# Kernel tuning notes

Measured on AMD Instinct MI355X. Metric: run time of the kernel, lower is better.

## Reference

```python
import jax, jax.numpy as jnp
import numpy as np

WS = 7      # window size
SS = 3      # shift size
NH = 6      # num heads
C = 192     # dim
B = 32
HH = 112
WW = 112


def _rel_pos_index(ws):
    coords = np.stack(np.meshgrid(np.arange(ws), np.arange(ws), indexing='ij'))
    cf = coords.reshape(2, -1)
    rel = (cf[:, :, None] - cf[:, None, :]).transpose(1, 2, 0)
    rel[:, :, 0] += ws - 1
    rel[:, :, 1] += ws - 1
    rel[:, :, 0] *= 2 * ws - 1
    return rel.sum(-1)  # (N, N) int


def _attn_mask(H, W, ws, ss):
    # standard Swin SW-MSA mask: -100 where tokens come from different regions
    img = np.zeros((H, W))
    cnt = 0
    for h in (slice(0, -ws), slice(-ws, -ss), slice(-ss, None)):
        for w in (slice(0, -ws), slice(-ws, -ss), slice(-ss, None)):
            img[h, w] = cnt
            cnt += 1
    mw = img.reshape(H // ws, ws, W // ws, ws).transpose(0, 2, 1, 3).reshape(-1, ws * ws)
    diff = mw[:, None, :] - mw[:, :, None]
    return np.where(diff != 0, -100.0, 0.0).astype(np.float32)  # (nW, N, N)


def _ln(x, g, b, eps=1e-5):
    m = x.mean(-1, keepdims=True)
    v = ((x - m) ** 2).mean(-1, keepdims=True)
    return (x - m) * jax.lax.rsqrt(v + eps) * g + b


def setup_inputs() -> dict:
    key = jax.random.key(0)
    ks = jax.random.split(key, 8)
    hid = 4 * C
    nbias = (2 * WS - 1) * (2 * WS - 1)
    return {
        'x': jax.random.normal(ks[0], (B, HH * WW, C), dtype=jnp.float32),
        'norm1_g': jnp.ones((C,), jnp.float32),
        'norm1_b': jnp.zeros((C,), jnp.float32),
        'qkv_w': jax.random.normal(ks[1], (3 * C, C), jnp.float32) * 0.02,
        'qkv_b': jnp.zeros((3 * C,), jnp.float32),
        'rpb_table': jax.random.normal(ks[2], (nbias, NH), jnp.float32) * 0.02,
        'proj_w': jax.random.normal(ks[3], (C, C), jnp.float32) * 0.02,
        'proj_b': jnp.zeros((C,), jnp.float32),
        'norm2_g': jnp.ones((C,), jnp.float32),
        'norm2_b': jnp.zeros((C,), jnp.float32),
        'fc1_w': jax.random.normal(ks[4], (hid, C), jnp.float32) * 0.02,
        'fc1_b': jnp.zeros((hid,), jnp.float32),
        'fc2_w': jax.random.normal(ks[5], (C, hid), jnp.float32) * 0.02,
        'fc2_b': jnp.zeros((C,), jnp.float32),
        'H': HH,
        'W': WW,
    }


def reference(x, norm1_g, norm1_b, qkv_w, qkv_b, rpb_table, proj_w, proj_b,
              norm2_g, norm2_b, fc1_w, fc1_b, fc2_w, fc2_b, H, W):
    Bb, L, Cc = x.shape
    N = WS * WS
    hd = Cc // NH
    rpi = jnp.asarray(_rel_pos_index(WS))                      # (N, N)
    amask = jnp.asarray(_attn_mask(H, W, WS, SS))              # (nW, N, N)
    nW = amask.shape[0]

    shortcut = x
    h = _ln(x, norm1_g, norm1_b).reshape(Bb, H, W, Cc)
    # cyclic shift
    h = jnp.roll(h, shift=(-SS, -SS), axis=(1, 2))
    # window partition -> (B*nW, N, C)
    h = h.reshape(Bb, H // WS, WS, W // WS, WS, Cc).transpose(0, 1, 3, 2, 4, 5)
    xw = h.reshape(-1, N, Cc)
    Bn = xw.shape[0]

    qkv = (xw @ qkv_w.T + qkv_b).reshape(Bn, N, 3, NH, hd).transpose(2, 0, 3, 1, 4)
    q, k, v = qkv[0], qkv[1], qkv[2]                           # (Bn, NH, N, hd)
    q = q * (hd ** -0.5)
    attn = jnp.einsum('bhnd,bhmd->bhnm', q, k)                 # (Bn, NH, N, N)
    bias = rpb_table[rpi.reshape(-1)].reshape(N, N, NH).transpose(2, 0, 1)
    attn = attn + bias[None]
    attn = (attn.reshape(Bb, nW, NH, N, N) + amask[None, :, None]).reshape(Bn, NH, N, N)
    attn = jax.nn.softmax(attn, axis=-1)
    out = jnp.einsum('bhnm,bhmd->bhnd', attn, v).transpose(0, 2, 1, 3).reshape(Bn, N, Cc)
    out = out @ proj_w.T + proj_b

    # window reverse + reverse cyclic shift
    out = out.reshape(Bb, H // WS, W // WS, WS, WS, Cc).transpose(0, 1, 3, 2, 4, 5).reshape(Bb, H, W, Cc)
    out = jnp.roll(out, shift=(SS, SS), axis=(1, 2)).reshape(Bb, L, Cc)

    x = shortcut + out
    y = _ln(x, norm2_g, norm2_b)
    y = jax.nn.gelu(y @ fc1_w.T + fc1_b, approximate=False) @ fc2_w.T + fc2_b
    return x + y
```

## Files before the change

### kernel.cpp

```cpp
#include <hip/hip_runtime.h>
#include <stdint.h>
#include <math.h>


typedef unsigned short u16;
typedef unsigned int   u32;
typedef __bf16 v8bf __attribute__((ext_vector_type(8)));
typedef float  v4f  __attribute__((ext_vector_type(4)));
typedef u16    v8u16 __attribute__((ext_vector_type(8)));
typedef u16    v4u16 __attribute__((ext_vector_type(4)));

#define MFMA16(a,b,c) __builtin_amdgcn_mfma_f32_16x16x32_bf16(a,b,c,0,0,0)

#define HSTR 77070336L
#define QSC  0.17677669529663687f

__device__ __forceinline__ u16 f2bf(float f){
  return __builtin_bit_cast(u16, (__bf16)f);
}

__device__ __forceinline__ void async16(void* lds, const void* g){
  __builtin_amdgcn_global_load_lds(
      (__attribute__((address_space(1))) void*)(g),
      (__attribute__((address_space(3))) void*)(lds), 16, 0, 0);
}

__global__ __launch_bounds__(256)
void convw(const float* __restrict__ s0, const float* __restrict__ s1,
           const float* __restrict__ s2, const float* __restrict__ s3,
           u16* __restrict__ d){
  int i = blockIdx.x * 256 + threadIdx.x;
  float v;
  if (i < 110592){
    v = s0[i];
    if (i < 36864) v *= QSC;
  }
  else if (i < 147456)  v = s1[i - 110592];
  else if (i < 294912)  v = s2[i - 147456];
  else                  v = s3[i - 294912];
  d[i] = f2bf(v);
}

__global__ __launch_bounds__(256)
void bmt_k(const float* __restrict__ rpb, float* __restrict__ bmt){
  int idx = blockIdx.x * 256 + threadIdx.x;
  int r  = idx & 3, lg = (idx >> 2) & 3, lr = (idx >> 4) & 15;
  int n  = (idx >> 8) & 3, m = (idx >> 10) & 3;
  int t  = idx >> 12; int h = t % 6, cls = t / 6;
  int row = m*16 + lg*4 + r, col = n*16 + lr;
  float v;
  if (row >= 49 || col >= 49){
    v = -1e30f;
  } else {
    int i1 = row / 7, j1 = row - i1 * 7;
    int i2 = col / 7, j2 = col - i2 * 7;
    int ridx = (i1 - i2 + 6) * 13 + (j1 - j2 + 6);
    v = rpb[ridx * 6 + h];
    int lh1 = (cls & 2) ? (i1 < 4 ? 1 : 2) : 0;
    int lw1 = (cls & 1) ? (j1 < 4 ? 1 : 2) : 0;
    int lh2 = (cls & 2) ? (i2 < 4 ? 1 : 2) : 0;
    int lw2 = (cls & 1) ? (j2 < 4 ? 1 : 2) : 0;
    if (lh1 * 3 + lw1 != lh2 * 3 + lw2) v -= 100.f;
  }
  bmt[idx] = v;
}

template<bool GATHER>
__global__ __launch_bounds__(256)
void ln_kern(const float* __restrict__ x, const float* __restrict__ g,
             const float* __restrict__ b, u16* __restrict__ o){
  const int ts  = threadIdx.x >> 4;
  const int l16 = threadIdx.x & 15;
  const int r   = blockIdx.x * 16 + ts;
  const float* src;
  if (GATHER){
    u32 wdx = (u32)r / 49u; int nn = r - (int)wdx * 49;
    int bb = (int)(wdx >> 8); int wl = (int)(wdx & 255);
    int wh = wl >> 4, wwi = wl & 15;
    int ii = (int)((u32)nn / 7u), jj = nn - ii * 7;
    int th = wh * 7 + ii + 3;  if (th >= 112) th -= 112;
    int tw = wwi * 7 + jj + 3; if (tw >= 112) tw -= 112;
    src = x + (u32)(bb * 12544 + th * 112 + tw) * 192u;
  } else {
    src = x + (u32)r * 192u;
  }
  const float4 a0 = *(const float4*)(src + l16*12);
  const float4 a1 = *(const float4*)(src + l16*12 + 4);
  const float4 a2 = *(const float4*)(src + l16*12 + 8);
  float sm = ((a0.x+a0.y)+(a0.z+a0.w)) + ((a1.x+a1.y)+(a1.z+a1.w))
           + ((a2.x+a2.y)+(a2.z+a2.w));
  float sq = ((a0.x*a0.x+a0.y*a0.y)+(a0.z*a0.z+a0.w*a0.w))
           + ((a1.x*a1.x+a1.y*a1.y)+(a1.z*a1.z+a1.w*a1.w))
           + ((a2.x*a2.x+a2.y*a2.y)+(a2.z*a2.z+a2.w*a2.w));
  #pragma unroll
  for (int d = 1; d < 16; d <<= 1){
    sm += __shfl_xor(sm, d, 64);
    sq += __shfl_xor(sq, d, 64);
  }
  float mean = sm * (1.f/192.f);
  float var  = sq * (1.f/192.f) - mean * mean;
  float rs   = rsqrtf(var + 1e-5f);
  const float4 g0 = *(const float4*)(g + l16*12);
  const float4 g1 = *(const float4*)(g + l16*12 + 4);
  const float4 g2 = *(const float4*)(g + l16*12 + 8);
  const float4 b0 = *(const float4*)(b + l16*12);
  const float4 b1 = *(const float4*)(b + l16*12 + 4);
  const float4 b2 = *(const float4*)(b + l16*12 + 8);
  u16* dst = o + (u32)r * 192u + l16 * 12;
  v4u16 w0, w1, w2;
  w0[0]=f2bf((a0.x-mean)*rs*g0.x+b0.x); w0[1]=f2bf((a0.y-mean)*rs*g0.y+b0.y);
  w0[2]=f2bf((a0.z-mean)*rs*g0.z+b0.z); w0[3]=f2bf((a0.w-mean)*rs*g0.w+b0.w);
  w1[0]=f2bf((a1.x-mean)*rs*g1.x+b1.x); w1[1]=f2bf((a1.y-mean)*rs*g1.y+b1.y);
  w1[2]=f2bf((a1.z-mean)*rs*g1.z+b1.z); w1[3]=f2bf((a1.w-mean)*rs*g1.w+b1.w);
  w2[0]=f2bf((a2.x-mean)*rs*g2.x+b2.x); w2[1]=f2bf((a2.y-mean)*rs*g2.y+b2.y);
  w2[2]=f2bf((a2.z-mean)*rs*g2.z+b2.z); w2[3]=f2bf((a2.w-mean)*rs*g2.w+b2.w);
  *(v4u16*)(dst)     = w0;
  *(v4u16*)(dst + 4) = w1;
  *(v4u16*)(dst + 8) = w2;
}

template<int EPI, int LDA, int LDW>
__global__ __launch_bounds__(512)
void gemm_bt(const u16* __restrict__ A, int aRowOff,
             const u16* __restrict__ W, int K, int ncol,
             const float* __restrict__ bias,
             u16* __restrict__ ob, float* __restrict__ of,
             const float* __restrict__ xres, int oRowOff){
  constexpr bool TRN = (EPI == 0);
  __shared__ __align__(16) u16 sA[128 * 200];
  __shared__ __align__(16) u16 sW[64 * 200];
  const int tid = threadIdx.x;
  const int wv = tid >> 6, lnn = tid & 63;
  const int lr = lnn & 15, lg = lnn >> 4;
  const int win = 56 * ncol;
  const int grp = (int)blockIdx.x / win, loc = (int)blockIdx.x - grp * win;
  const int rloc = loc % 56, cblk = loc / 56;
  const int m0   = (grp * 56 + rloc) * 128;
  const int col0 = cblk * 64;
  const int wr = wv >> 1, wc = wv & 1;

  const int c0   = col0 + wc*32 + lr;
  const int chb0 = col0 + wc*32 + lg*4;
  const int chb1 = chb0 + 16;

  v4f acc[2][2];
  if (TRN){
    float4 bv0 = *(const float4*)&bias[chb0];
    float4 bv1 = *(const float4*)&bias[chb1];
    if (chb0 < 192){ bv0.x*=QSC; bv0.y*=QSC; bv0.z*=QSC; bv0.w*=QSC; }
    if (chb1 < 192){ bv1.x*=QSC; bv1.y*=QSC; bv1.z*=QSC; bv1.w*=QSC; }
    acc[0][0] = acc[0][1] = (v4f){bv0.x, bv0.y, bv0.z, bv0.w};
    acc[1][0] = acc[1][1] = (v4f){bv1.x, bv1.y, bv1.z, bv1.w};
  } else {
    const float b0v = bias[c0];
    const float b1v = bias[c0 + 16];
    #pragma unroll
    for (int m = 0; m < 2; ++m){
      acc[m][0] = (v4f){b0v, b0v, b0v, b0v};
      acc[m][1] = (v4f){b1v, b1v, b1v, b1v};
    }
  }

  const int rA0 = (int)((u32)tid / 25u);
  const int cA0 = tid - rA0 * 25;
  const u32 aBase = (u32)(aRowOff + m0);
  const int nK = K / 192;
  for (int ks = 0; ks < nK; ++ks){
    if (ks) __syncthreads();
    const int k0 = ks * 192;
    int ra = rA0, ca = cA0;
    #pragma unroll
    for (int it = 0; it < 6; ++it){
      int cc = (ca == 24) ? 23 : ca;
      async16((char*)sA + (size_t)(it * 512 + wv * 64) * 16,
              A + (aBase + (u32)ra) * (u32)LDA + (u32)(k0 + cc * 8));
      ra += 20; ca += 12; if (ca >= 25){ ca -= 25; ra += 1; }
    }
    if (tid < 128){
      int cc = (ca == 24) ? 23 : ca;
      async16((char*)sA + (size_t)(3072 + wv * 64) * 16,
              A + (aBase + (u32)ra) * (u32)LDA + (u32)(k0 + cc * 8));
    }
    int rw = rA0, cw = cA0;
    #pragma unroll
    for (int it = 0; it < 3; ++it){
      int cc = (cw == 24) ? 23 : cw;
      async16((char*)sW + (size_t)(it * 512 + wv * 64) * 16,
              W + (u32)(col0 + rw) * (u32)LDW + (u32)(k0 + cc * 8));
      rw += 20; cw += 12; if (cw >= 25){ cw -= 25; rw += 1; }
    }
    if (tid < 64){
      int cc = (cw == 24) ? 23 : cw;
      async16((char*)sW + (size_t)1536 * 16,
              W + (u32)(col0 + rw) * (u32)LDW + (u32)(k0 + cc * 8));
    }
    __syncthreads();

    #pragma unroll
    for (int kk = 0; kk < 6; ++kk){
      v8bf af[2], wf[2];
      #pragma unroll
      for (int m = 0; m < 2; ++m)
        af[m] = *(const v8bf*)&sA[(wr*32 + m*16 + lr) * 200 + kk*32 + lg*8];
      #pragma unroll
      for (int n = 0; n < 2; ++n)
        wf[n] = *(const v8bf*)&sW[(wc*32 + n*16 + lr) * 200 + kk*32 + lg*8];
      if (TRN){
        #pragma unroll
        for (int n = 0; n < 2; ++n)
          #pragma unroll
          for (int m = 0; m < 2; ++m)
            acc[n][m] = MFMA16(wf[n], af[m], acc[n][m]);
      } else {
        #pragma unroll
        for (int m = 0; m < 2; ++m)
          #pragma unroll
          for (int n = 0; n < 2; ++n)
            acc[m][n] = MFMA16(af[m], wf[n], acc[m][n]);
      }
    }
  }

  if (EPI == 0){
    u32 chpart[2];
    const int chbs[2] = {chb0, chb1};
    #pragma unroll
    for (int n = 0; n < 2; ++n){
      int ch = chbs[n];
      int which = (ch >= 384) ? 2 : ((ch >= 192) ? 1 : 0);
      int rem = ch - which * 192;
      chpart[n] = (u32)which * 77070336u + (u32)((rem >> 5) * 1568 + (rem & 31));
    }
    #pragma unroll
    for (int m = 0; m < 2; ++m){
      const int t = m0 + wr*32 + m*16 + lr;
      u32 wdx = (u32)t / 49u; u32 tnn = (u32)t - wdx * 49u;
      const u32 rowpart = wdx * 9408u + tnn * 32u;
      #pragma unroll
      for (int n = 0; n < 2; ++n){
        v4u16 pk;
        pk[0] = f2bf(acc[n][m][0]); pk[1] = f2bf(acc[n][m][1]);
        pk[2] = f2bf(acc[n][m][2]); pk[3] = f2bf(acc[n][m][3]);
        *(v4u16*)&ob[chpart[n] + rowpart] = pk;
      }
    }
  } else if (EPI == 1){
    #pragma unroll
    for (int m = 0; m < 2; ++m){
      #pragma unroll
      for (int r = 0; r < 4; ++r){
        const int gr = m0 + wr*32 + m*16 + lg*4 + r;
        u32 wdx = (u32)gr / 49u; int nn = gr - (int)wdx * 49;
        int bb = (int)(wdx >> 8); int wl = (int)(wdx & 255);
        int wh = wl >> 4, wwi = wl & 15;
        int ii = (int)((u32)nn / 7u), jj = nn - ii * 7;
        int th = wh * 7 + ii + 3;  if (th >= 112) th -= 112;
        int tw = wwi * 7 + jj + 3; if (tw >= 112) tw -= 112;
        u32 adr = (u32)(bb * 12544 + th * 112 + tw) * 192u + (u32)c0;
        of[adr]      = xres[adr]      + acc[m][0][r];
        of[adr + 16] = xres[adr + 16] + acc[m][1][r];
      }
    }
  } else if (EPI == 3){
    #pragma unroll
    for (int m = 0; m < 2; ++m){
      #pragma unroll
      for (int r = 0; r < 4; ++r){
        const u32 adr = (u32)(oRowOff + m0 + wr*32 + m*16 + lg*4 + r) * 192u
                        + (u32)c0;
        of[adr]      += acc[m][0][r];
        of[adr + 16] += acc[m][1][r];
      }
    }
  } else {
    #pragma unroll
    for (int m = 0; m < 2; ++m){
      #pragma unroll
      for (int r = 0; r < 4; ++r){
        const u32 base = (u32)(m0 + wr*32 + m*16 + lg*4 + r) * 768u + (u32)c0;
        float v0 = acc[m][0][r], v1 = acc[m][1][r];
        ob[base]      = f2bf(0.5f * v0 * (1.0f + erff(v0 * 0.7071067811865475f)));
        ob[base + 16] = f2bf(0.5f * v1 * (1.0f + erff(v1 * 0.7071067811865475f)));
      }
    }
  }
}

__global__ __launch_bounds__(256, 4)
void attn_k(const u16* __restrict__ qkv, const float* __restrict__ bmt,
            u16* __restrict__ aout){
  __shared__ __align__(16) u16 plds[4][64 * 64];
  const int wv = threadIdx.x >> 6, lnn = threadIdx.x & 63;
  const int lr = lnn & 15, lg = lnn >> 4;
  const u32 gid = (u32)blockIdx.x * 4u + (u32)wv;
  const u32 w = gid / 6u; const int h = (int)(gid - w * 6u);
  const u16* qb = qkv + (size_t)gid * 1568;
  const u16* kb = qb + HSTR;
  const u16* vb = kb + HSTR;

  const int wl = (int)(w & 255);
  const int cls = (((wl >> 4) == 15) ? 2 : 0) | (((wl & 15) == 15) ? 1 : 0);
  const float* bmv = bmt + ((u32)(cls * 6 + h) << 12);
  v4f s[4][4];
  #pragma unroll
  for (int m = 0; m < 4; ++m)
    #pragma unroll
    for (int n = 0; n < 4; ++n)
      s[m][n] = *(const v4f*)&bmv[(u32)(((m*4 + n)*16 + lr)*16 + lg*4)];

  v8bf aq[4], bk4[4];
  #pragma unroll
  for (int m = 0; m < 4; ++m) aq[m]  = *(const v8bf*)(qb + (m*16 + lr)*32 + lg*8);
  #pragma unroll
  for (int n = 0; n < 4; ++n) bk4[n] = *(const v8bf*)(kb + (n*16 + lr)*32 + lg*8);
  #pragma unroll
  for (int m = 0; m < 4; ++m)
    #pragma unroll
    for (int n = 0; n < 4; ++n) s[m][n] = MFMA16(aq[m], bk4[n], s[m][n]);

  v8u16 bvu[2][2];
  #pragma unroll
  for (int n2 = 0; n2 < 2; ++n2)
    #pragma unroll
    for (int ksi = 0; ksi < 2; ++ksi)
      #pragma unroll
      for (int e = 0; e < 8; ++e){
        int kp = ksi * 32 + lg * 8 + e;
        int t  = (kp >> 2) + (kp & 3) * 16;
        bvu[n2][ksi][e] = vb[(u32)(t * 32 + n2 * 16 + lr)];
      }

  #pragma unroll
  for (int m = 0; m < 4; ++m)
    #pragma unroll
    for (int r = 0; r < 4; ++r){
      int row = m*16 + lg*4 + r;
      v4u16 pk;
      pk[0] = f2bf(__expf(s[m][0][r]));
      pk[1] = f2bf(__expf(s[m][1][r]));
      pk[2] = f2bf(__expf(s[m][2][r]));
      pk[3] = f2bf(__expf(s[m][3][r]));
      *(v4u16*)((char*)&plds[wv][0] + row*128 + ((lr*8) ^ ((row & 7) << 4))) = pk;
    }

  v8bf pa[4][2];
  #pragma unroll
  for (int m2 = 0; m2 < 4; ++m2)
    #pragma unroll
    for (int ksi = 0; ksi < 2; ++ksi){
      int row2 = m2*16 + lr;
      pa[m2][ksi] = *(const v8bf*)((const char*)&plds[wv][0] + row2*128 +
                                   ((ksi*64 + lg*16) ^ ((row2 & 7) << 4)));
    }

  v8u16 onesu;
  #pragma unroll
  for (int e = 0; e < 8; ++e) onesu[e] = (lr == 0) ? (u16)0x3F80 : (u16)0;
  const v8bf onesf = __builtin_bit_cast(v8bf, onesu);

  const v4f zf = {0.f, 0.f, 0.f, 0.f};
  v4f o2[4][2], sacc[4];
  #pragma unroll
  for (int m2 = 0; m2 < 4; ++m2){
    o2[m2][0] = zf; o2[m2][1] = zf; sacc[m2] = zf;
  }
  #pragma unroll
  for (int ksi = 0; ksi < 2; ++ksi)
    #pragma unroll
    for (int m2 = 0; m2 < 4; ++m2){
      o2[m2][0] = MFMA16(pa[m2][ksi], __builtin_bit_cast(v8bf, bvu[0][ksi]), o2[m2][0]);
      o2[m2][1] = MFMA16(pa[m2][ksi], __builtin_bit_cast(v8bf, bvu[1][ksi]), o2[m2][1]);
      sacc[m2]  = MFMA16(pa[m2][ksi], onesf, sacc[m2]);
    }

  float inv[4][4];
  #pragma unroll
  for (int m2 = 0; m2 < 4; ++m2)
    #pragma unroll
    for (int r = 0; r < 4; ++r)
      inv[m2][r] = 1.0f / __shfl(sacc[m2][r], lnn & 48, 64);

  #pragma unroll
  for (int m2 = 0; m2 < 4; ++m2){
    #pragma unroll
    for (int n2 = 0; n2 < 2; ++n2){
      #pragma unroll
      for (int r = 0; r < 4; ++r){
        int row = m2*16 + lg*4 + r;
        if (row < 49){
          float val = o2[m2][n2][r] * inv[m2][r];
          aout[(w * 49u + (u32)row) * 192u + (u32)(h*32 + n2*16 + lr)] = f2bf(val);
        }
      }
    }
  }
}

extern "C" void kernel_launch(void* const* d_in, const int* in_sizes, int n_in,
                              void* d_out, int out_size, void* d_ws, size_t ws_size,
                              hipStream_t stream){
  const float* x     = (const float*)d_in[0];
  const float* n1g   = (const float*)d_in[1];
  const float* n1b   = (const float*)d_in[2];
  const float* qkvw  = (const float*)d_in[3];
  const float* qkvb  = (const float*)d_in[4];
  const float* rpb   = (const float*)d_in[5];
  const float* projw = (const float*)d_in[6];
  const float* projb = (const float*)d_in[7];
  const float* n2g   = (const float*)d_in[8];
  const float* n2b   = (const float*)d_in[9];
  const float* fc1w  = (const float*)d_in[10];
  const float* fc1b  = (const float*)d_in[11];
  const float* fc2w  = (const float*)d_in[12];
  const float* fc2b  = (const float*)d_in[13];
  float* out = (float*)d_out;

  char* ws  = (char*)d_ws;
  u16* bufA = (u16*)ws;
  u16* bufB = (u16*)(ws + 462422016L);
  u16* wq   = (u16*)(ws + 616562688L);
  u16* wp   = wq + 110592;
  u16* w1   = wp + 36864;
  u16* w2   = w1 + 147456;
  float* bmt = (float*)d_out;

  convw<<<1728, 256, 0, stream>>>(qkvw, projw, fc1w, fc2w, wq);
  bmt_k<<<384, 256, 0, stream>>>(rpb, bmt);

  ln_kern<true><<<25088, 256, 0, stream>>>(x, n1g, n1b, bufB);
  gemm_bt<0, 192, 192><<<3136*9, 512, 0, stream>>>(bufB, 0, wq, 192, 9,
                                                   qkvb, bufA, nullptr, nullptr, 0);
  attn_k<<<12288, 256, 0, stream>>>(bufA, bmt, bufB);
  gemm_bt<1, 192, 192><<<3136*3, 512, 0, stream>>>(bufB, 0, wp, 192, 3,
                                                   projb, nullptr, out, x, 0);
  ln_kern<false><<<25088, 256, 0, stream>>>(out, n2g, n2b, bufB);
  for (int c = 0; c < 2; ++c){
    int off = c * 200704;
    gemm_bt<2, 192, 192><<<1568*12, 512, 0, stream>>>(bufB, off, w1, 192, 12,
                                                      fc1b, bufA, nullptr, nullptr, 0);
    gemm_bt<3, 768, 768><<<1568*3, 512, 0, stream>>>(bufA, 0, w2, 768, 3,
                                                     fc2b, nullptr, out, nullptr, off);
  }
}
```

Baseline: 1.374 ms.

## Chunk QKV+attention and MLP into eight row slices to keep intermediates cache-resident

The QKV GEMM and window attention are split into eight batch chunks, so each chunk's QKV intermediate (about 58MB instead of 462MB) can stay in the large last-level cache before attention reads it. The head stride becomes a runtime parameter, and attention takes a window offset so mask class and output indexing stay global. The MLP loop goes from two to eight chunks so the fc1 hidden buffer also shrinks. The cost is more kernel launches, smaller grids per launch, and tail effects at each chunk boundary.

Result: no change. 1.349 ms (-1.8%).

```diff
diff --git a/kernel.cpp b/kernel.cpp
--- a/kernel.cpp
+++ b/kernel.cpp
@@ -12,7 +12,6 @@
 
 #define MFMA16(a,b,c) __builtin_amdgcn_mfma_f32_16x16x32_bf16(a,b,c,0,0,0)
 
-#define HSTR 77070336L
 #define QSC  0.17677669529663687f
 
 __device__ __forceinline__ u16 f2bf(float f){
@@ -125,7 +124,7 @@
              const u16* __restrict__ W, int K, int ncol,
              const float* __restrict__ bias,
              u16* __restrict__ ob, float* __restrict__ of,
-             const float* __restrict__ xres, int oRowOff){
+             const float* __restrict__ xres, int oRowOff, u32 hstr){
   constexpr bool TRN = (EPI == 0);
   __shared__ __align__(16) u16 sA[128 * 200];
   __shared__ __align__(16) u16 sW[64 * 200];
@@ -229,7 +228,7 @@
       int ch = chbs[n];
       int which = (ch >= 384) ? 2 : ((ch >= 192) ? 1 : 0);
       int rem = ch - which * 192;
-      chpart[n] = (u32)which * 77070336u + (u32)((rem >> 5) * 1568 + (rem & 31));
+      chpart[n] = (u32)which * hstr + (u32)((rem >> 5) * 1568 + (rem & 31));
     }
     #pragma unroll
     for (int m = 0; m < 2; ++m){
@@ -288,17 +287,18 @@
 
 __global__ __launch_bounds__(256, 4)
 void attn_k(const u16* __restrict__ qkv, const float* __restrict__ bmt,
-            u16* __restrict__ aout){
+            u16* __restrict__ aout, u32 wOff, u32 hstr){
   __shared__ __align__(16) u16 plds[4][64 * 64];
   const int wv = threadIdx.x >> 6, lnn = threadIdx.x & 63;
   const int lr = lnn & 15, lg = lnn >> 4;
   const u32 gid = (u32)blockIdx.x * 4u + (u32)wv;
   const u32 w = gid / 6u; const int h = (int)(gid - w * 6u);
   const u16* qb = qkv + (size_t)gid * 1568;
-  const u16* kb = qb + HSTR;
-  const u16* vb = kb + HSTR;
-
-  const int wl = (int)(w & 255);
+  const u16* kb = qb + hstr;
+  const u16* vb = kb + hstr;
+  const u32 wg = w + wOff;
+
+  const int wl = (int)(wg & 255u);
   const int cls = (((wl >> 4) == 15) ? 2 : 0) | (((wl & 15) == 15) ? 1 : 0);
   const float* bmv = bmt + ((u32)(cls * 6 + h) << 12);
   v4f s[4][4];
@@ -389,7 +389,7 @@
         int row = m2*16 + lg*4 + r;
         if (row < 49){
           float val = o2[m2][n2][r] * inv[m2][r];
-          aout[(w * 49u + (u32)row) * 192u + (u32)(h*32 + n2*16 + lr)] = f2bf(val);
+          aout[(wg * 49u + (u32)row) * 192u + (u32)(h*32 + n2*16 + lr)] = f2bf(val);
         }
       }
     }
@@ -428,17 +428,27 @@
   bmt_k<<<384, 256, 0, stream>>>(rpb, bmt);
 
   ln_kern<true><<<25088, 256, 0, stream>>>(x, n1g, n1b, bufB);
-  gemm_bt<0, 192, 192><<<3136*9, 512, 0, stream>>>(bufB, 0, wq, 192, 9,
-                                                   qkvb, bufA, nullptr, nullptr, 0);
-  attn_k<<<12288, 256, 0, stream>>>(bufA, bmt, bufB);
+
+  const u32 HC = 9633792u;
+  for (int c = 0; c < 8; ++c){
+    const int rowOff = c * 50176;
+    gemm_bt<0, 192, 192><<<392*9, 512, 0, stream>>>(bufB, rowOff, wq, 192, 9,
+                                                    qkvb, bufA, nullptr,
+                                                    nullptr, 0, HC);
+    attn_k<<<1536, 256, 0, stream>>>(bufA, bmt, bufB, (u32)(c * 1024), HC);
+  }
+
   gemm_bt<1, 192, 192><<<3136*3, 512, 0, stream>>>(bufB, 0, wp, 192, 3,
-                                                   projb, nullptr, out, x, 0);
+                                                   projb, nullptr, out, x, 0, 0);
   ln_kern<false><<<25088, 256, 0, stream>>>(out, n2g, n2b, bufB);
-  for (int c = 0; c < 2; ++c){
-    int off = c * 200704;
-    gemm_bt<2, 192, 192><<<1568*12, 512, 0, stream>>>(bufB, off, w1, 192, 12,
-                                                      fc1b, bufA, nullptr, nullptr, 0);
-    gemm_bt<3, 768, 768><<<1568*3, 512, 0, stream>>>(bufA, 0, w2, 768, 3,
-                                                     fc2b, nullptr, out, nullptr, off);
-  }
-}
+
+  for (int c = 0; c < 8; ++c){
+    const int off = c * 50176;
+    gemm_bt<2, 192, 192><<<392*12, 512, 0, stream>>>(bufB, off, w1, 192, 12,
+                                                     fc1b, bufA, nullptr,
+                                                     nullptr, 0, 0);
+    gemm_bt<3, 768, 768><<<392*3, 512, 0, stream>>>(bufA, 0, w2, 768, 3,
+                                                    fc2b, nullptr, out,
+                                                    nullptr, off, 0);
+  }
+}
```
